# Optimization experiments

Measured on AMD Instinct MI355X. Metric: run time of the kernel, lower is better.

The kernel has to match this reference:

```python
import jax, jax.numpy as jnp
import numpy as np
import math

B, L, IN, HID, NLAYERS, AA = 16, 512, 512, 512, 6, 21
KAPPA_ADD = 5.0


def _sru_layer(x, W, v, b):
    # x: [L, B, din]; W: [din, 2*HID*k]; v, b: [2(gate f/r), 2(dir), HID]
    Lx, Bx, din = x.shape
    d = HID
    k = W.shape[1] // (2 * d)  # 4 if projecting residual, 3 if residual = input
    U = (x @ W).reshape(Lx, Bx, 2, d, k)
    res = U[..., 3] if k == 4 else x.reshape(Lx, Bx, 2, d)
    # time-flip direction 1 so a single scan handles both directions
    flip = lambda a: jnp.concatenate([a[:, :, :1], a[::-1, :, 1:]], axis=2)
    u0, u1, u2, resf = flip(U[..., 0]), flip(U[..., 1]), flip(U[..., 2]), flip(res)
    vf, vr = v[0], v[1]
    bf, br = b[0], b[1]

    def step(c, t):
        u0t, u1t, u2t, rt = t
        f = jax.nn.sigmoid(u1t + vf * c + bf)
        c1 = f * c + (1.0 - f) * u0t
        r = jax.nn.sigmoid(u2t + vr * c1 + br)
        h = r * c1 + (1.0 - r) * rt
        return c1, h

    c0 = jnp.zeros((Bx, 2, d), x.dtype)
    _, H = jax.lax.scan(step, c0, (u0, u1, u2, resf))
    return flip(H).reshape(Lx, Bx, 2 * d)


def setup_inputs():
    key = jax.random.key(0)
    inp = {}
    inp['input'] = jax.random.normal(jax.random.fold_in(key, 0), (B, L, IN), jnp.float32)
    inp['hidden'] = jnp.zeros((NLAYERS, B, 2 * HID), jnp.float32)
    for l in range(NLAYERS):
        din = IN if l == 0 else 2 * HID
        k = 4 if din != 2 * HID else 3
        inp[f'sru_w{l}'] = jax.random.normal(jax.random.fold_in(key, 10 + l), (din, 2 * HID * k), jnp.float32) * (1.0 / math.sqrt(din))
        inp[f'sru_v{l}'] = jax.random.normal(jax.random.fold_in(key, 20 + l), (2, 2, HID), jnp.float32) * 0.1
        inp[f'sru_b{l}'] = jnp.zeros((2, 2, HID), jnp.float32)

    def lin(seed, din, dout):
        w = jax.random.normal(jax.random.fold_in(key, seed), (din, dout), jnp.float32) * (1.0 / math.sqrt(din))
        return w, jnp.zeros((dout,), jnp.float32)

    inp['fc1_logits_w'], inp['fc1_logits_b'] = lin(30, 2 * HID, HID)
    inp['fc2_logits_w'], inp['fc2_logits_b'] = lin(31, HID, AA)
    inp['fc1_angles_w'], inp['fc1_angles_b'] = lin(32, 2 * HID, HID)
    inp['fc2_means_w'], inp['fc2_means_b'] = lin(33, HID, 2)
    inp['fc2_kappas_w'], inp['fc2_kappas_b'] = lin(34, HID, 2)
    return inp


def reference(input, hidden, sru_w0, sru_v0, sru_b0, sru_w1, sru_v1, sru_b1, sru_w2, sru_v2, sru_b2, sru_w3, sru_v3, sru_b3, sru_w4, sru_v4, sru_b4, sru_w5, sru_v5, sru_b5, fc1_logits_w, fc1_logits_b, fc2_logits_w, fc2_logits_b, fc1_angles_w, fc1_angles_b, fc2_means_w, fc2_means_b, fc2_kappas_w, fc2_kappas_b):
    x = input.transpose(1, 0, 2)  # [L, B, IN]
    ws = [sru_w0, sru_w1, sru_w2, sru_w3, sru_w4, sru_w5]
    vs = [sru_v0, sru_v1, sru_v2, sru_v3, sru_v4, sru_v5]
    bs = [sru_b0, sru_b1, sru_b2, sru_b3, sru_b4, sru_b5]
    for W, v, b in zip(ws, vs, bs):
        x = _sru_layer(x, W, v, b)
    sru_out = x.transpose(1, 0, 2)  # [B, L, 2*HID]
    h_log = sru_out @ fc1_logits_w + fc1_logits_b
    output_logits = jax.nn.log_softmax(h_log @ fc2_logits_w + fc2_logits_b, axis=-1)
    h_ang = sru_out @ fc1_angles_w + fc1_angles_b
    output_means = jnp.tanh(h_ang @ fc2_means_w + fc2_means_b) * math.pi
    output_kappas = KAPPA_ADD + jax.nn.softplus(h_ang @ fc2_kappas_w + fc2_kappas_b)
    return (output_logits, output_means, output_kappas)
```

## Files before the change

### kernel.cpp

```cpp
#include <hip/hip_runtime.h>

typedef __attribute__((ext_vector_type(8))) short short8;
typedef __attribute__((ext_vector_type(4))) float f32x4;

__device__ __forceinline__ ushort f2bf(float x) {
  unsigned u = __builtin_bit_cast(unsigned, x);
  u = (u + 0x7fffu + ((u >> 16) & 1u)) >> 16;
  return (ushort)u;
}
__device__ __forceinline__ float bf2f(ushort x) {
  return __builtin_bit_cast(float, ((unsigned)x) << 16);
}

#define AS1CP(p) ((const __attribute__((address_space(1))) unsigned int*)(p))
#define AS3CP(p) ((__attribute__((address_space(3))) unsigned int*)(p))
#define GLDS(g, l, SZ) __builtin_amdgcn_global_load_lds(AS1CP(g), AS3CP(l), SZ, 0, 0)

__global__ __launch_bounds__(256) void k_cvt(const float* __restrict__ in,
                                             ushort* __restrict__ out, int n4) {
  int i = blockIdx.x * 256 + threadIdx.x;
  if (i >= n4) return;
  float4 v = reinterpret_cast<const float4*>(in)[i];
  ushort4 o;
  o.x = f2bf(v.x); o.y = f2bf(v.y); o.z = f2bf(v.z); o.w = f2bf(v.w);
  reinterpret_cast<ushort4*>(out)[i] = o;
}

__global__ __launch_bounds__(256) void k_transpose(const float* __restrict__ W,
                                                   ushort* __restrict__ Wt,
                                                   int N, int K) {
  __shared__ float tile[32][33];
  int bx = blockIdx.x * 32;
  int by = blockIdx.y * 32;
  int tx = threadIdx.x, ty = threadIdx.y;
#pragma unroll
  for (int i = 0; i < 32; i += 8)
    tile[ty + i][tx] = W[(size_t)(by + ty + i) * N + bx + tx];
  __syncthreads();
#pragma unroll
  for (int i = 0; i < 32; i += 8)
    Wt[(size_t)(bx + ty + i) * K + by + tx] = f2bf(tile[tx][ty + i]);
}

template <int KKp>
__global__ __launch_bounds__(256) void k_transpose_sru(const float* __restrict__ W,
                                                       ushort* __restrict__ Wt,
                                                       int N, int K) {
  __shared__ float tile[32][33];
  int bx = blockIdx.x * 32;
  int by = blockIdx.y * 32;
  int tx = threadIdx.x, ty = threadIdx.y;
#pragma unroll
  for (int i = 0; i < 32; i += 8)
    tile[ty + i][tx] = W[(size_t)(by + ty + i) * N + bx + tx];
  __syncthreads();
#pragma unroll
  for (int i = 0; i < 32; i += 8) {
    int c = bx + ty + i;
    int ch = c / KKp, j = c - ch * KKp;
    int nc = (j < 2) ? (ch * 2 + j) : ((j == 2) ? (2048 + ch) : (3072 + ch));
    Wt[(size_t)nc * K + by + tx] = f2bf(tile[tx][ty + i]);
  }
}

template <int BF16OUT>
__global__ __launch_bounds__(256) void k_gemm(const ushort* __restrict__ A,
                                              const ushort* __restrict__ Bt,
                                              void* __restrict__ Cv,
                                              int K, int N) {
  __shared__ __align__(16) ushort lsA[2][4096];
  __shared__ __align__(16) ushort lsB[2][4096];
  const int tid = threadIdx.x;
  const int bm = blockIdx.x, bn = blockIdx.y;
  const int w = tid >> 6, l = tid & 63;
  const int wm = (w >> 1) * 64, wn = (w & 1) * 64;
  const int lr = l & 15, lg = l >> 4;
  f32x4 acc[4][4] = {};
  const int srow = tid >> 2;
  const int scol = (((tid & 3) ^ ((srow >> 1) & 3))) * 8;
  const ushort* Ag = A + (size_t)(bm * 128 + srow) * K + scol;
  const ushort* Bg = Bt + (size_t)(bn * 128 + srow) * K + scol;
  const int nt = K >> 5;
  const int rxor = (lr >> 1) & 3;

#define GEMM_ISSUE(BUF, KT)                                       \
  {                                                               \
    GLDS(Ag + (KT), &lsA[BUF][w * 512], 16);                      \
    GLDS(Ag + (size_t)64 * K + (KT), &lsA[BUF][2048 + w * 512], 16); \
    GLDS(Bg + (KT), &lsB[BUF][w * 512], 16);                      \
    GLDS(Bg + (size_t)64 * K + (KT), &lsB[BUF][2048 + w * 512], 16); \
  }

  GEMM_ISSUE(0, 0);
  for (int t = 0; t < nt; ++t) {
    const int cur = t & 1;
    if (t + 1 < nt) {
      GEMM_ISSUE(cur ^ 1, (t + 1) * 32);
      asm volatile("s_waitcnt vmcnt(4)" ::: "memory");
    } else {
      asm volatile("s_waitcnt vmcnt(0)" ::: "memory");
    }
    asm volatile("s_barrier" ::: "memory");
    short8 af[4], bfr[4];
#pragma unroll
    for (int i = 0; i < 4; ++i)
      af[i] = *(const short8*)&lsA[cur][(wm + i * 16 + lr) * 32 + ((lg ^ rxor) * 8)];
#pragma unroll
    for (int j = 0; j < 4; ++j)
      bfr[j] = *(const short8*)&lsB[cur][(wn + j * 16 + lr) * 32 + ((lg ^ rxor) * 8)];
#pragma unroll
    for (int i = 0; i < 4; ++i)
#pragma unroll
      for (int j = 0; j < 4; ++j)
        acc[i][j] = __builtin_amdgcn_mfma_f32_16x16x32_bf16(af[i], bfr[j], acc[i][j], 0, 0, 0);
    asm volatile("s_barrier" ::: "memory");
  }
#undef GEMM_ISSUE
  const size_t cbase = (size_t)(bm * 128 + wm + lg * 4) * N + bn * 128 + wn + lr;
  if (BF16OUT) {
    ushort* Cb = (ushort*)Cv + cbase;
#pragma unroll
    for (int i = 0; i < 4; ++i)
#pragma unroll
      for (int j = 0; j < 4; ++j)
#pragma unroll
        for (int r = 0; r < 4; ++r)
          Cb[(size_t)(i * 16 + r) * N + j * 16] = f2bf(acc[i][j][r]);
  } else {
    float* Cb = (float*)Cv + cbase;
#pragma unroll
    for (int i = 0; i < 4; ++i)
#pragma unroll
      for (int j = 0; j < 4; ++j)
#pragma unroll
        for (int r = 0; r < 4; ++r)
          Cb[(size_t)(i * 16 + r) * N + j * 16] = acc[i][j][r];
  }
}

__global__ __launch_bounds__(64, 1) void sru_rec8(const ushort* __restrict__ U, int NU,
                                                  const ushort* __restrict__ R, int RS,
                                                  const float* __restrict__ v,
                                                  const float* __restrict__ bb,
                                                  ushort* __restrict__ H) {
  const int lane = threadIdx.x;
  const int blk = blockIdx.x;
  const int b = blk >> 4, rem = blk & 15, dir = rem >> 3, cg = rem & 7;
  const int ch = dir * 512 + cg * 64 + lane;
  const float vf = v[ch], vr = v[1024 + ch];
  const float bfv = bb[ch], brv = bb[1024 + ch];
  const float vfn = -vf, vrn = -vr;
  const float kf0 = -bfv, kr0 = -brv;
  const int tstep = dir ? -1 : 1;
  const int t0 = dir ? 511 : 0;
  const ushort* U01 = U + (size_t)b * 512 * NU + ch * 2;
  const ushort* U2  = U + (size_t)b * 512 * NU + 2048 + ch;
  const ushort* Rb  = R + (size_t)b * 512 * RS + ch;
  ushort* Hb = H + (size_t)b * 512 * 1024 + ch;

  unsigned q01[4][8];
  ushort q2[4][8], qr[4][8];

#define SR_ISSUE(J, TI)                                                        \
  {                                                                            \
    const int base_ = (TI) * 8;                                                \
    _Pragma("unroll")                                                          \
    for (int t = 0; t < 8; ++t) {                                              \
      int tt = t0 + tstep * (base_ + t);                                       \
      q01[J][t] = *(const unsigned*)(U01 + (size_t)tt * NU);                   \
      q2[J][t] = U2[(size_t)tt * NU];                                          \
      qr[J][t] = Rb[(size_t)tt * RS];                                          \
    }                                                                          \
  }

#define SR_COMP(J, TI)                                                         \
  {                                                                            \
    _Pragma("unroll")                                                          \
    for (int s = 0; s < 8; ++s) {                                              \
      float u0 = __builtin_bit_cast(float, q01[J][s] << 16);                   \
      float u1 = __builtin_bit_cast(float, q01[J][s] & 0xffff0000u);           \
      float u2 = bf2f(q2[J][s]);                                               \
      float uR = bf2f(qr[J][s]);                                               \
      float ef = __expf(__builtin_fmaf(vfn, c, kf0 - u1));                     \
      float f = __builtin_amdgcn_rcpf(1.f + ef);                               \
      c = __builtin_fmaf(f, c - u0, u0);                                       \
      float er = __expf(__builtin_fmaf(vrn, c, kr0 - u2));                     \
      float r = __builtin_amdgcn_rcpf(1.f + er);                               \
      float hh = __builtin_fmaf(r, c - uR, uR);                                \
      Hb[(size_t)(t0 + tstep * ((TI) * 8 + s)) * 1024] = f2bf(hh);             \
    }                                                                          \
  }

  SR_ISSUE(0, 0)
  SR_ISSUE(1, 1)
  SR_ISSUE(2, 2)
  float c = 0.f;
#pragma unroll 1
  for (int ii = 0; ii < 15; ++ii) {
#define TILE_J(J)                                                              \
    {                                                                          \
      const int i = ii * 4 + (J);                                              \
      SR_ISSUE((((J) + 3) & 3), i + 3)                                         \
      asm volatile("s_waitcnt vmcnt(63)" ::: "memory");                        \
      SR_COMP(J, i)                                                            \
    }
    TILE_J(0) TILE_J(1) TILE_J(2) TILE_J(3)
#undef TILE_J
  }
  SR_ISSUE(3, 63)
  asm volatile("s_waitcnt vmcnt(63)" ::: "memory");
  SR_COMP(0, 60)
  asm volatile("s_waitcnt vmcnt(48)" ::: "memory");
  SR_COMP(1, 61)
  asm volatile("s_waitcnt vmcnt(24)" ::: "memory");
  SR_COMP(2, 62)
  asm volatile("s_waitcnt vmcnt(0)" ::: "memory");
  SR_COMP(3, 63)
#undef SR_ISSUE
#undef SR_COMP
}

__global__ __launch_bounds__(256) void k_buildW2(const float* __restrict__ w2l,
                                                 const float* __restrict__ w2m,
                                                 const float* __restrict__ w2k,
                                                 ushort* __restrict__ Wt2) {
  int i = blockIdx.x * 256 + threadIdx.x;
  if (i >= 128 * 1024) return;
  int n = i >> 10, k = i & 1023;
  float vv = 0.f;
  if (n < 21 && k < 512) vv = w2l[k * 21 + n];
  else if (n >= 21 && n < 23 && k >= 512) vv = w2m[(k - 512) * 2 + (n - 21)];
  else if (n >= 23 && n < 25 && k >= 512) vv = w2k[(k - 512) * 2 + (n - 23)];
  Wt2[i] = f2bf(vv);
}

__global__ __launch_bounds__(64) void k_bias25(const float* __restrict__ b1l,
                                               const float* __restrict__ b1a,
                                               const float* __restrict__ w2l,
                                               const float* __restrict__ b2l,
                                               const float* __restrict__ w2m,
                                               const float* __restrict__ b2m,
                                               const float* __restrict__ w2k,
                                               const float* __restrict__ b2k,
                                               float* __restrict__ b2adj) {
  int o = threadIdx.x;
  if (o >= 25) return;
  float s;
  if (o < 21) {
    s = b2l[o];
    for (int k = 0; k < 512; ++k) s += b1l[k] * w2l[k * 21 + o];
  } else if (o < 23) {
    s = b2m[o - 21];
    for (int k = 0; k < 512; ++k) s += b1a[k] * w2m[k * 2 + (o - 21)];
  } else {
    s = b2k[o - 23];
    for (int k = 0; k < 512; ++k) s += b1a[k] * w2k[k * 2 + (o - 23)];
  }
  b2adj[o] = s;
}

__global__ __launch_bounds__(64) void k_act(const float* __restrict__ T,
                                            const float* __restrict__ b2adj,
                                            float* __restrict__ out) {
  const int row = blockIdx.x;
  const int lane = threadIdx.x;
  float myv = 0.f;
  if (lane < 25) myv = T[(size_t)row * 128 + lane] + b2adj[lane];
  float x = (lane < 21) ? myv : -1e30f;
#pragma unroll
  for (int off = 32; off; off >>= 1) x = fmaxf(x, __shfl_xor(x, off));
  float e = (lane < 21) ? expf(myv - x) : 0.f;
#pragma unroll
  for (int off = 32; off; off >>= 1) e += __shfl_xor(e, off);
  float lse = x + logf(e);
  if (lane < 21) {
    out[(size_t)row * 21 + lane] = myv - lse;
  } else if (lane < 23) {
    out[172032 + row * 2 + (lane - 21)] = tanhf(myv) * 3.14159265358979323846f;
  } else if (lane < 25) {
    float sp = (myv > 20.f) ? myv : log1pf(expf(myv));
    out[188416 + row * 2 + (lane - 23)] = 5.f + sp;
  }
}

extern "C" void kernel_launch(void* const* d_in, const int* in_sizes, int n_in,
                              void* d_out, int out_size, void* d_ws, size_t ws_size,
                              hipStream_t stream) {
  (void)in_sizes; (void)n_in; (void)out_size; (void)ws_size;
  const float* input = (const float*)d_in[0];
  const float* sw[6]; const float* sv[6]; const float* sb[6];
  for (int l = 0; l < 6; ++l) {
    sw[l] = (const float*)d_in[2 + 3 * l];
    sv[l] = (const float*)d_in[3 + 3 * l];
    sb[l] = (const float*)d_in[4 + 3 * l];
  }
  const float* fc1lw = (const float*)d_in[20];
  const float* fc1lb = (const float*)d_in[21];
  const float* fc2lw = (const float*)d_in[22];
  const float* fc2lb = (const float*)d_in[23];
  const float* fc1aw = (const float*)d_in[24];
  const float* fc1ab = (const float*)d_in[25];
  const float* fc2mw = (const float*)d_in[26];
  const float* fc2mb = (const float*)d_in[27];
  const float* fc2kw = (const float*)d_in[28];
  const float* fc2kb = (const float*)d_in[29];

  char* ws = (char*)d_ws;
  ushort* U = (ushort*)ws;
  ushort* Hcat2 = (ushort*)ws;
  float* T = (float*)(ws + 67108864);
  ushort* H0 = (ushort*)(ws + 134217728);
  ushort* H1 = (ushort*)(ws + 150994944);
  ushort* X0 = (ushort*)(ws + 167772160);
  const size_t wbase = 176160768;
  ushort* Wtl[6];
  Wtl[0] = (ushort*)(ws + wbase);
  for (int l = 1; l < 6; ++l)
    Wtl[l] = (ushort*)(ws + wbase + 4194304 + (size_t)(l - 1) * 6291456);
  ushort* Wfc = (ushort*)(ws + wbase + 4194304 + 5ull * 6291456);
  ushort* Wt2 = (ushort*)(ws + wbase + 37748736);
  float* b2adj = (float*)(ws + wbase + 38010880);

  k_cvt<<<4096, 256, 0, stream>>>(input, X0, 8192 * 512 / 4);
  k_buildW2<<<512, 256, 0, stream>>>(fc2lw, fc2mw, fc2kw, Wt2);
  k_bias25<<<1, 64, 0, stream>>>(fc1lb, fc1ab, fc2lw, fc2lb, fc2mw, fc2mb,
                                 fc2kw, fc2kb, b2adj);

  k_transpose_sru<4><<<dim3(128, 16), dim3(32, 8), 0, stream>>>(sw[0], Wtl[0], 4096, 512);
  for (int l = 1; l < 6; ++l)
    k_transpose_sru<3><<<dim3(96, 32), dim3(32, 8), 0, stream>>>(sw[l], Wtl[l], 3072, 1024);
  k_transpose<<<dim3(16, 32), dim3(32, 8), 0, stream>>>(fc1lw, Wfc, 512, 1024);
  k_transpose<<<dim3(16, 32), dim3(32, 8), 0, stream>>>(fc1aw, Wfc + (size_t)512 * 1024, 512, 1024);

  for (int l = 0; l < 6; ++l) {
    const ushort* Ain = (l == 0) ? X0 : ((l & 1) ? H0 : H1);
    ushort* Hout = (l & 1) ? H1 : H0;
    int K = (l == 0) ? 512 : 1024;
    int N = (l == 0) ? 4096 : 3072;
    k_gemm<1><<<dim3(64, N / 128), 256, 0, stream>>>(Ain, Wtl[l], U, K, N);
    if (l == 0)
      sru_rec8<<<256, 64, 0, stream>>>(U, 4096, U + 3072, 4096, sv[l], sb[l], Hout);
    else
      sru_rec8<<<256, 64, 0, stream>>>(U, 3072, Ain, 1024, sv[l], sb[l], Hout);
  }

  k_gemm<1><<<dim3(64, 8), 256, 0, stream>>>(H1, Wfc, Hcat2, 1024, 1024);

  k_gemm<0><<<dim3(64, 1), 256, 0, stream>>>(Hcat2, Wt2, T, 1024, 128);

  k_act<<<8192, 64, 0, stream>>>(T, b2adj, (float*)d_out);
}
```

Measured before the change: 769.6 us.

## Interleave SRU gate projections per channel and deepen GEMM LDS pipeline

The SRU recurrence now reads u0,u1,u2 and the residual for each channel as one 8-byte load from an interleaved [t][ch][4] buffer, instead of three separate strided loads from U and the previous layer's output. The recurrence also writes its output into slot 3 of the next layer's U buffer, and the GEMM gains a mode that scatters columns into that interleaved layout. The GEMM's LDS ring grows from two to four stages so more loads stay in flight. The costs are strided 2-byte scatter stores in the GEMM epilogue, an extra store per step in the recurrence, double-buffered U workspace, and four times the LDS per block, which may reduce occupancy.

```diff
diff --git a/kernel.cpp b/kernel.cpp
--- a/kernel.cpp
+++ b/kernel.cpp
@@ -2,6 +2,7 @@
 
 typedef __attribute__((ext_vector_type(8))) short short8;
 typedef __attribute__((ext_vector_type(4))) float f32x4;
+typedef __attribute__((ext_vector_type(2))) unsigned uint2v;
 
 __device__ __forceinline__ ushort f2bf(float x) {
   unsigned u = __builtin_bit_cast(unsigned, x);
@@ -42,34 +43,13 @@
     Wt[(size_t)(bx + ty + i) * K + by + tx] = f2bf(tile[tx][ty + i]);
 }
 
-template <int KKp>
-__global__ __launch_bounds__(256) void k_transpose_sru(const float* __restrict__ W,
-                                                       ushort* __restrict__ Wt,
-                                                       int N, int K) {
-  __shared__ float tile[32][33];
-  int bx = blockIdx.x * 32;
-  int by = blockIdx.y * 32;
-  int tx = threadIdx.x, ty = threadIdx.y;
-#pragma unroll
-  for (int i = 0; i < 32; i += 8)
-    tile[ty + i][tx] = W[(size_t)(by + ty + i) * N + bx + tx];
-  __syncthreads();
-#pragma unroll
-  for (int i = 0; i < 32; i += 8) {
-    int c = bx + ty + i;
-    int ch = c / KKp, j = c - ch * KKp;
-    int nc = (j < 2) ? (ch * 2 + j) : ((j == 2) ? (2048 + ch) : (3072 + ch));
-    Wt[(size_t)nc * K + by + tx] = f2bf(tile[tx][ty + i]);
-  }
-}
-
-template <int BF16OUT>
+template <int MODE>
 __global__ __launch_bounds__(256) void k_gemm(const ushort* __restrict__ A,
                                               const ushort* __restrict__ Bt,
                                               void* __restrict__ Cv,
                                               int K, int N) {
-  __shared__ __align__(16) ushort lsA[2][4096];
-  __shared__ __align__(16) ushort lsB[2][4096];
+  __shared__ __align__(16) ushort lsA[4][4096];
+  __shared__ __align__(16) ushort lsB[4][4096];
   const int tid = threadIdx.x;
   const int bm = blockIdx.x, bn = blockIdx.y;
   const int w = tid >> 6, l = tid & 63;
@@ -83,22 +63,27 @@
   const int nt = K >> 5;
   const int rxor = (lr >> 1) & 3;
 
-#define GEMM_ISSUE(BUF, KT)                                       \
-  {                                                               \
-    GLDS(Ag + (KT), &lsA[BUF][w * 512], 16);                      \
-    GLDS(Ag + (size_t)64 * K + (KT), &lsA[BUF][2048 + w * 512], 16); \
-    GLDS(Bg + (KT), &lsB[BUF][w * 512], 16);                      \
-    GLDS(Bg + (size_t)64 * K + (KT), &lsB[BUF][2048 + w * 512], 16); \
+#define GEMM_ISSUE(SL, KT)                                          \
+  {                                                                 \
+    GLDS(Ag + (KT), &lsA[SL][w * 512], 16);                         \
+    GLDS(Ag + (size_t)64 * K + (KT), &lsA[SL][2048 + w * 512], 16); \
+    GLDS(Bg + (KT), &lsB[SL][w * 512], 16);                         \
+    GLDS(Bg + (size_t)64 * K + (KT), &lsB[SL][2048 + w * 512], 16); \
   }
 
   GEMM_ISSUE(0, 0);
+  GEMM_ISSUE(1, 32);
+  GEMM_ISSUE(2, 64);
   for (int t = 0; t < nt; ++t) {
-    const int cur = t & 1;
-    if (t + 1 < nt) {
-      GEMM_ISSUE(cur ^ 1, (t + 1) * 32);
-      asm volatile("s_waitcnt vmcnt(4)" ::: "memory");
+    const int cur = t & 3;
+    if (t + 3 < nt) {
+      GEMM_ISSUE((t + 3) & 3, (t + 3) * 32);
+      asm volatile("s_waitcnt vmcnt(12)" ::: "memory");
     } else {
-      asm volatile("s_waitcnt vmcnt(0)" ::: "memory");
+      const int rem = nt - 1 - t;
+      if (rem == 2)      asm volatile("s_waitcnt vmcnt(8)" ::: "memory");
+      else if (rem == 1) asm volatile("s_waitcnt vmcnt(4)" ::: "memory");
+      else               asm volatile("s_waitcnt vmcnt(0)" ::: "memory");
     }
     asm volatile("s_barrier" ::: "memory");
     short8 af[4], bfr[4];
@@ -116,9 +101,22 @@
     asm volatile("s_barrier" ::: "memory");
   }
 #undef GEMM_ISSUE
-  const size_t cbase = (size_t)(bm * 128 + wm + lg * 4) * N + bn * 128 + wn + lr;
-  if (BF16OUT) {
-    ushort* Cb = (ushort*)Cv + cbase;
+  const int row0 = bm * 128 + wm + lg * 4;
+  if (MODE == 2) {
+    ushort* Cb = (ushort*)Cv;
+#pragma unroll
+    for (int j = 0; j < 4; ++j) {
+      unsigned n = bn * 128 + wn + j * 16 + lr;
+      unsigned c2 = n / 3u;
+      unsigned col = c2 * 4 + (n - c2 * 3u);
+#pragma unroll
+      for (int i = 0; i < 4; ++i)
+#pragma unroll
+        for (int r = 0; r < 4; ++r)
+          Cb[(size_t)(row0 + i * 16 + r) * 4096 + col] = f2bf(acc[i][j][r]);
+    }
+  } else if (MODE == 1) {
+    ushort* Cb = (ushort*)Cv + (size_t)row0 * N + bn * 128 + wn + lr;
 #pragma unroll
     for (int i = 0; i < 4; ++i)
 #pragma unroll
@@ -127,7 +125,7 @@
         for (int r = 0; r < 4; ++r)
           Cb[(size_t)(i * 16 + r) * N + j * 16] = f2bf(acc[i][j][r]);
   } else {
-    float* Cb = (float*)Cv + cbase;
+    float* Cb = (float*)Cv + (size_t)row0 * N + bn * 128 + wn + lr;
 #pragma unroll
     for (int i = 0; i < 4; ++i)
 #pragma unroll
@@ -138,28 +136,27 @@
   }
 }
 
-__global__ __launch_bounds__(64, 1) void sru_rec8(const ushort* __restrict__ U, int NU,
-                                                  const ushort* __restrict__ R, int RS,
+template <int WRITE_NEXT>
+__global__ __launch_bounds__(64, 1) void sru_rec9(const ushort* __restrict__ U,
                                                   const float* __restrict__ v,
                                                   const float* __restrict__ bb,
-                                                  ushort* __restrict__ H) {
+                                                  ushort* __restrict__ H,
+                                                  ushort* __restrict__ Un) {
   const int lane = threadIdx.x;
   const int blk = blockIdx.x;
   const int b = blk >> 4, rem = blk & 15, dir = rem >> 3, cg = rem & 7;
-  const int ch = dir * 512 + cg * 64 + lane;
-  const float vf = v[ch], vr = v[1024 + ch];
-  const float bfv = bb[ch], brv = bb[1024 + ch];
+  const int c2 = dir * 512 + cg * 64 + lane;
+  const float vf = v[c2], vr = v[1024 + c2];
+  const float bfv = bb[c2], brv = bb[1024 + c2];
   const float vfn = -vf, vrn = -vr;
   const float kf0 = -bfv, kr0 = -brv;
   const int tstep = dir ? -1 : 1;
   const int t0 = dir ? 511 : 0;
-  const ushort* U01 = U + (size_t)b * 512 * NU + ch * 2;
-  const ushort* U2  = U + (size_t)b * 512 * NU + 2048 + ch;
-  const ushort* Rb  = R + (size_t)b * 512 * RS + ch;
-  ushort* Hb = H + (size_t)b * 512 * 1024 + ch;
-
-  unsigned q01[4][8];
-  ushort q2[4][8], qr[4][8];
+  const ushort* Ub = U + (size_t)b * 512 * 4096 + c2 * 4;
+  ushort* Hb = H + (size_t)b * 512 * 1024 + c2;
+  ushort* Unb = Un + (size_t)b * 512 * 4096 + c2 * 4 + 3;
+
+  uint2v q[4][8];
 
 #define SR_ISSUE(J, TI)                                                        \
   {                                                                            \
@@ -167,9 +164,7 @@
     _Pragma("unroll")                                                          \
     for (int t = 0; t < 8; ++t) {                                              \
       int tt = t0 + tstep * (base_ + t);                                       \
-      q01[J][t] = *(const unsigned*)(U01 + (size_t)tt * NU);                   \
-      q2[J][t] = U2[(size_t)tt * NU];                                          \
-      qr[J][t] = Rb[(size_t)tt * RS];                                          \
+      q[J][t] = *(const uint2v*)(Ub + (size_t)tt * 4096);                      \
     }                                                                          \
   }
 
@@ -177,17 +172,21 @@
   {                                                                            \
     _Pragma("unroll")                                                          \
     for (int s = 0; s < 8; ++s) {                                              \
-      float u0 = __builtin_bit_cast(float, q01[J][s] << 16);                   \
-      float u1 = __builtin_bit_cast(float, q01[J][s] & 0xffff0000u);           \
-      float u2 = bf2f(q2[J][s]);                                               \
-      float uR = bf2f(qr[J][s]);                                               \
+      unsigned lo = q[J][s].x, hi = q[J][s].y;                                 \
+      float u0 = __builtin_bit_cast(float, lo << 16);                          \
+      float u1 = __builtin_bit_cast(float, lo & 0xffff0000u);                  \
+      float u2 = __builtin_bit_cast(float, hi << 16);                          \
+      float uR = __builtin_bit_cast(float, hi & 0xffff0000u);                  \
       float ef = __expf(__builtin_fmaf(vfn, c, kf0 - u1));                     \
       float f = __builtin_amdgcn_rcpf(1.f + ef);                               \
       c = __builtin_fmaf(f, c - u0, u0);                                       \
       float er = __expf(__builtin_fmaf(vrn, c, kr0 - u2));                     \
       float r = __builtin_amdgcn_rcpf(1.f + er);                               \
       float hh = __builtin_fmaf(r, c - uR, uR);                                \
-      Hb[(size_t)(t0 + tstep * ((TI) * 8 + s)) * 1024] = f2bf(hh);             \
+      ushort hb = f2bf(hh);                                                    \
+      int tt = t0 + tstep * ((TI) * 8 + s);                                    \
+      Hb[(size_t)tt * 1024] = hb;                                              \
+      if (WRITE_NEXT) Unb[(size_t)tt * 4096] = hb;                             \
     }                                                                          \
   }
 
@@ -201,18 +200,18 @@
     {                                                                          \
       const int i = ii * 4 + (J);                                              \
       SR_ISSUE((((J) + 3) & 3), i + 3)                                         \
-      asm volatile("s_waitcnt vmcnt(63)" ::: "memory");                        \
+      asm volatile("s_waitcnt vmcnt(24)" ::: "memory");                        \
       SR_COMP(J, i)                                                            \
     }
     TILE_J(0) TILE_J(1) TILE_J(2) TILE_J(3)
 #undef TILE_J
   }
   SR_ISSUE(3, 63)
-  asm volatile("s_waitcnt vmcnt(63)" ::: "memory");
+  asm volatile("s_waitcnt vmcnt(24)" ::: "memory");
   SR_COMP(0, 60)
-  asm volatile("s_waitcnt vmcnt(48)" ::: "memory");
+  asm volatile("s_waitcnt vmcnt(16)" ::: "memory");
   SR_COMP(1, 61)
-  asm volatile("s_waitcnt vmcnt(24)" ::: "memory");
+  asm volatile("s_waitcnt vmcnt(8)" ::: "memory");
   SR_COMP(2, 62)
   asm volatile("s_waitcnt vmcnt(0)" ::: "memory");
   SR_COMP(3, 63)
@@ -306,9 +305,10 @@
   const float* fc2kb = (const float*)d_in[29];
 
   char* ws = (char*)d_ws;
-  ushort* U = (ushort*)ws;
+  ushort* Ua = (ushort*)ws;
+  ushort* Ubf = (ushort*)(ws + 67108864);
   ushort* Hcat2 = (ushort*)ws;
-  float* T = (float*)(ws + 67108864);
+  float* T = (float*)(ws + 33554432);
   ushort* H0 = (ushort*)(ws + 134217728);
   ushort* H1 = (ushort*)(ws + 150994944);
   ushort* X0 = (ushort*)(ws + 167772160);
@@ -326,22 +326,26 @@
   k_bias25<<<1, 64, 0, stream>>>(fc1lb, fc1ab, fc2lw, fc2lb, fc2mw, fc2mb,
                                  fc2kw, fc2kb, b2adj);
 
-  k_transpose_sru<4><<<dim3(128, 16), dim3(32, 8), 0, stream>>>(sw[0], Wtl[0], 4096, 512);
+  k_transpose<<<dim3(128, 16), dim3(32, 8), 0, stream>>>(sw[0], Wtl[0], 4096, 512);
   for (int l = 1; l < 6; ++l)
-    k_transpose_sru<3><<<dim3(96, 32), dim3(32, 8), 0, stream>>>(sw[l], Wtl[l], 3072, 1024);
+    k_transpose<<<dim3(96, 32), dim3(32, 8), 0, stream>>>(sw[l], Wtl[l], 3072, 1024);
   k_transpose<<<dim3(16, 32), dim3(32, 8), 0, stream>>>(fc1lw, Wfc, 512, 1024);
   k_transpose<<<dim3(16, 32), dim3(32, 8), 0, stream>>>(fc1aw, Wfc + (size_t)512 * 1024, 512, 1024);
 
+  ushort* Ucur = Ua;
+  ushort* Unxt = Ubf;
   for (int l = 0; l < 6; ++l) {
     const ushort* Ain = (l == 0) ? X0 : ((l & 1) ? H0 : H1);
     ushort* Hout = (l & 1) ? H1 : H0;
-    int K = (l == 0) ? 512 : 1024;
-    int N = (l == 0) ? 4096 : 3072;
-    k_gemm<1><<<dim3(64, N / 128), 256, 0, stream>>>(Ain, Wtl[l], U, K, N);
     if (l == 0)
-      sru_rec8<<<256, 64, 0, stream>>>(U, 4096, U + 3072, 4096, sv[l], sb[l], Hout);
+      k_gemm<1><<<dim3(64, 32), 256, 0, stream>>>(Ain, Wtl[0], Ucur, 512, 4096);
     else
-      sru_rec8<<<256, 64, 0, stream>>>(U, 3072, Ain, 1024, sv[l], sb[l], Hout);
+      k_gemm<2><<<dim3(64, 24), 256, 0, stream>>>(Ain, Wtl[l], Ucur, 1024, 3072);
+    if (l < 5)
+      sru_rec9<1><<<256, 64, 0, stream>>>(Ucur, sv[l], sb[l], Hout, Unxt);
+    else
+      sru_rec9<0><<<256, 64, 0, stream>>>(Ucur, sv[l], sb[l], Hout, Unxt);
+    ushort* tmp = Ucur; Ucur = Unxt; Unxt = tmp;
   }
 
   k_gemm<1><<<dim3(64, 8), 256, 0, stream>>>(H1, Wfc, Hcat2, 1024, 1024);
```

Measured after the change: 859.7 us. 1.12x slower.

## Use 256x256 tiled 8-wave GEMM with split-K staging for SRU projections

Applied to the files above, without the earlier changes.

Adds a new GEMM kernel with 256x256 output tiles, 512 threads and a 64-wide K step split into two 32-wide halves. The second half's loads are issued between the two MFMA phases. MFMA issue priority is raised with s_setprio. The larger tile gives more operand reuse and fewer global loads per FLOP, at the cost of fewer blocks (e.g. 384 for N=3072, 128 for the fc1 GEMM) and one block per CU, which may underfill the 256 CUs. The small final GEMM keeps the old kernel.

```diff
diff --git a/kernel.cpp b/kernel.cpp
--- a/kernel.cpp
+++ b/kernel.cpp
@@ -64,10 +64,110 @@
 }
 
 template <int BF16OUT>
-__global__ __launch_bounds__(256) void k_gemm(const ushort* __restrict__ A,
-                                              const ushort* __restrict__ Bt,
-                                              void* __restrict__ Cv,
-                                              int K, int N) {
+__global__ __launch_bounds__(512, 1) void k_gemm256(const ushort* __restrict__ A,
+                                                    const ushort* __restrict__ Bt,
+                                                    void* __restrict__ Cv,
+                                                    int K, int N) {
+  __shared__ __align__(16) ushort lsA[2][2][8192];
+  __shared__ __align__(16) ushort lsB[2][2][8192];
+  const int tid = threadIdx.x;
+  const int bm = blockIdx.x, bn = blockIdx.y;
+  const int w = tid >> 6, lane = tid & 63;
+  const int wm = (w >> 2) * 128, wn = (w & 3) * 64;
+  const int lr = lane & 15, lg = lane >> 4;
+  const int rx = (lr >> 1) & 3;
+  f32x4 acc[8][4] = {};
+  const int swk = ((lane & 3) ^ ((lane >> 3) & 3)) * 8;
+  const ushort* Asrc = A + (size_t)(bm * 256 + w * 32 + (lane >> 2)) * K + swk;
+  const ushort* Bsrc = Bt + (size_t)(bn * 256 + w * 32 + (lane >> 2)) * K + swk;
+  const int nt = K >> 6;
+
+#define STAGE_HALF(BUF, KT, S)                                            \
+  {                                                                       \
+    GLDS(Asrc + (KT) + (S) * 32, &lsA[BUF][S][w * 1024], 16);             \
+    GLDS(Asrc + (size_t)16 * K + (KT) + (S) * 32, &lsA[BUF][S][w * 1024 + 512], 16); \
+    GLDS(Bsrc + (KT) + (S) * 32, &lsB[BUF][S][w * 1024], 16);             \
+    GLDS(Bsrc + (size_t)16 * K + (KT) + (S) * 32, &lsB[BUF][S][w * 1024 + 512], 16); \
+  }
+
+  STAGE_HALF(0, 0, 0);
+  STAGE_HALF(0, 0, 1);
+  asm volatile("s_waitcnt vmcnt(0)" ::: "memory");
+  asm volatile("s_barrier" ::: "memory");
+
+  for (int t = 0; t < nt; ++t) {
+    const int cur = t & 1;
+    const int nb = cur ^ 1;
+    if (t + 1 < nt) {
+      STAGE_HALF(nb, (t + 1) * 64, 0);
+      asm volatile("s_waitcnt vmcnt(4)" ::: "memory");
+    } else {
+      asm volatile("s_waitcnt vmcnt(0)" ::: "memory");
+    }
+    asm volatile("s_barrier" ::: "memory");
+    {
+      short8 af[8], bf[4];
+#pragma unroll
+      for (int i = 0; i < 8; ++i)
+        af[i] = *(const short8*)&lsA[cur][0][(wm + i * 16 + lr) * 32 + (lg ^ rx) * 8];
+#pragma unroll
+      for (int j = 0; j < 4; ++j)
+        bf[j] = *(const short8*)&lsB[cur][0][(wn + j * 16 + lr) * 32 + (lg ^ rx) * 8];
+      __builtin_amdgcn_s_setprio(1);
+#pragma unroll
+      for (int i = 0; i < 8; ++i)
+#pragma unroll
+        for (int j = 0; j < 4; ++j)
+          acc[i][j] = __builtin_amdgcn_mfma_f32_16x16x32_bf16(af[i], bf[j], acc[i][j], 0, 0, 0);
+      __builtin_amdgcn_s_setprio(0);
+    }
+    if (t + 1 < nt) STAGE_HALF(nb, (t + 1) * 64, 1);
+    {
+      short8 af[8], bf[4];
+#pragma unroll
+      for (int i = 0; i < 8; ++i)
+        af[i] = *(const short8*)&lsA[cur][1][(wm + i * 16 + lr) * 32 + (lg ^ rx) * 8];
+#pragma unroll
+      for (int j = 0; j < 4; ++j)
+        bf[j] = *(const short8*)&lsB[cur][1][(wn + j * 16 + lr) * 32 + (lg ^ rx) * 8];
+      __builtin_amdgcn_s_setprio(1);
+#pragma unroll
+      for (int i = 0; i < 8; ++i)
+#pragma unroll
+        for (int j = 0; j < 4; ++j)
+          acc[i][j] = __builtin_amdgcn_mfma_f32_16x16x32_bf16(af[i], bf[j], acc[i][j], 0, 0, 0);
+      __builtin_amdgcn_s_setprio(0);
+    }
+    asm volatile("s_barrier" ::: "memory");
+  }
+#undef STAGE_HALF
+  const size_t cbase = (size_t)(bm * 256 + wm + lg * 4) * N + bn * 256 + wn + lr;
+  if (BF16OUT) {
+    ushort* Cb = (ushort*)Cv + cbase;
+#pragma unroll
+    for (int i = 0; i < 8; ++i)
+#pragma unroll
+      for (int j = 0; j < 4; ++j)
+#pragma unroll
+        for (int r = 0; r < 4; ++r)
+          Cb[(size_t)(i * 16 + r) * N + j * 16] = f2bf(acc[i][j][r]);
+  } else {
+    float* Cb = (float*)Cv + cbase;
+#pragma unroll
+    for (int i = 0; i < 8; ++i)
+#pragma unroll
+      for (int j = 0; j < 4; ++j)
+#pragma unroll
+        for (int r = 0; r < 4; ++r)
+          Cb[(size_t)(i * 16 + r) * N + j * 16] = acc[i][j][r];
+  }
+}
+
+template <int BF16OUT>
+__global__ __launch_bounds__(256) void k_gemm_s(const ushort* __restrict__ A,
+                                                const ushort* __restrict__ Bt,
+                                                void* __restrict__ Cv,
+                                                int K, int N) {
   __shared__ __align__(16) ushort lsA[2][4096];
   __shared__ __align__(16) ushort lsB[2][4096];
   const int tid = threadIdx.x;
@@ -83,11 +183,11 @@
   const int nt = K >> 5;
   const int rxor = (lr >> 1) & 3;
 
-#define GEMM_ISSUE(BUF, KT)                                       \
-  {                                                               \
-    GLDS(Ag + (KT), &lsA[BUF][w * 512], 16);                      \
+#define GEMM_ISSUE(BUF, KT)                                          \
+  {                                                                  \
+    GLDS(Ag + (KT), &lsA[BUF][w * 512], 16);                         \
     GLDS(Ag + (size_t)64 * K + (KT), &lsA[BUF][2048 + w * 512], 16); \
-    GLDS(Bg + (KT), &lsB[BUF][w * 512], 16);                      \
+    GLDS(Bg + (KT), &lsB[BUF][w * 512], 16);                         \
     GLDS(Bg + (size_t)64 * K + (KT), &lsB[BUF][2048 + w * 512], 16); \
   }
 
@@ -337,16 +437,16 @@
     ushort* Hout = (l & 1) ? H1 : H0;
     int K = (l == 0) ? 512 : 1024;
     int N = (l == 0) ? 4096 : 3072;
-    k_gemm<1><<<dim3(64, N / 128), 256, 0, stream>>>(Ain, Wtl[l], U, K, N);
+    k_gemm256<1><<<dim3(32, N / 256), 512, 0, stream>>>(Ain, Wtl[l], U, K, N);
     if (l == 0)
       sru_rec8<<<256, 64, 0, stream>>>(U, 4096, U + 3072, 4096, sv[l], sb[l], Hout);
     else
       sru_rec8<<<256, 64, 0, stream>>>(U, 3072, Ain, 1024, sv[l], sb[l], Hout);
   }
 
-  k_gemm<1><<<dim3(64, 8), 256, 0, stream>>>(H1, Wfc, Hcat2, 1024, 1024);
-
-  k_gemm<0><<<dim3(64, 1), 256, 0, stream>>>(Hcat2, Wt2, T, 1024, 128);
+  k_gemm256<1><<<dim3(32, 4), 512, 0, stream>>>(H1, Wfc, Hcat2, 1024, 1024);
+
+  k_gemm_s<0><<<dim3(64, 1), 256, 0, stream>>>(Hcat2, Wt2, T, 1024, 128);
 
   k_act<<<8192, 64, 0, stream>>>(T, b2adj, (float*)d_out);
 }
```

After: 851.5 us. 1.11x slower.
